# Kernel tuning notes

Hardware: AMD Instinct MI355X
Metric: run time of the kernel (lower is better)

Reference implementation:

```python
import jax, jax.numpy as jnp
import numpy as np
import math

# ---- constants derived from PCF.__init__(nbbins=50, sigma=0.25, npoints=1024, n_rmax=5) ----
NBBINS = 50
SIGMA = 0.25
NPOINTS = 1024
N_RMAX = 5
RMAX = float(2.0 * np.sqrt(1.0 / (2.0 * np.sqrt(3.0) * NPOINTS)))
_STEP = N_RMAX / NBBINS
RS = np.array([(i + 1) * _STEP * RMAX for i in range(NBBINS)], dtype=np.float32)
AREA = np.array([math.pi * ((r + 0.5 * RMAX) ** 2 - max(0.0, r - 0.5 * RMAX) ** 2) for r in RS],
                dtype=np.float32)
GF = float(1.0 / (np.sqrt(math.pi) * SIGMA))


def _gaussian_kernel(x):
    return GF * jnp.exp(-(x * x) / (SIGMA * SIGMA))


def _perimeter_weight(x, y, rs):
    """x, y: [N] disk centers in [0,1]^2; rs: [B]. Returns [N, B] inverse in-domain perimeter fraction."""
    full = jnp.full((x.shape[0], rs.shape[0]), 2.0 * math.pi, dtype=x.dtype)

    def corr(full_angle, dx, dy):
        # dx, dy: [N] distance to a domain edge (as in the four blocks of perimeter_weight)
        mask = rs[None, :] > dx[:, None]                       # [N, B]
        alpha = jnp.arccos(jnp.clip(dx[:, None] / rs[None, :], -1.0, 1.0))
        sub = (jnp.minimum(alpha, jnp.arctan2(dy, dx)[:, None])
               + jnp.minimum(alpha, jnp.arctan2(1.0 - dy, dx)[:, None]))
        return full_angle - jnp.where(mask, sub, 0.0)

    full = corr(full, x, y)          # left edge
    full = corr(full, 1.0 - x, y)    # right edge
    full = corr(full, y, x)          # bottom edge
    full = corr(full, 1.0 - y, x)    # top edge
    peri = jnp.clip(full / (2.0 * math.pi), 0.0, 1.0)
    pos = peri > 0
    return jnp.where(pos, 1.0 / jnp.where(pos, peri, 1.0), 0.0)


def _disk_distance(pa, pb, rmax):
    """pa: [Na,3], pb: [Nb,3] disks (x, y, r) -> pairwise disk distance [Na, Nb] (repo utils.diskDistance)."""
    diff = pa[:, None, 0:2] - pb[None, :, 0:2]
    d = jnp.sqrt(jnp.sum(diff * diff, axis=-1))                # [Na, Nb]
    ra = pa[:, 2][:, None]
    rb = pb[None, :, 2]
    r1 = jnp.maximum(ra, rb)
    r2 = jnp.minimum(ra, rb)
    extent = jnp.maximum(d + r1 + r2, 2.0 * r1)
    overlap = jnp.clip(r1 + r2 - d, 0.0, None)
    return (extent - overlap + d + r1 - r2) / rmax


def _pcf_forward(disks_a, disks_b, same_category):
    rs = jnp.asarray(RS)
    area = jnp.asarray(AREA)
    na = disks_a.shape[0]
    nb = disks_b.shape[0]
    dist = _disk_distance(disks_a, disks_b, RMAX)              # [Na, Nb]
    # val[i, j, b] = gauss(rs_b / rmax - dist_ij)
    val = _gaussian_kernel(rs[None, None, :] / RMAX - dist[:, :, None])  # [Na, Nb, B]
    if same_category:
        # exclude self-pair j == i (torch.cat of slices around i)
        eye = jnp.eye(na, nb, dtype=val.dtype)
        val = val * (1.0 - eye)[:, :, None]
    contrib = jnp.sum(val, axis=1)                             # [Na, B]
    weights = _perimeter_weight(disks_a[:, 0], disks_a[:, 1], rs)  # [Na, B] (diskfact = 1/domainLength = 1)
    density = contrib * weights / area[None, :] / nb           # [Na, B]
    pcf_mean = jnp.sum(density, axis=0) / na                   # [B]
    pcf_lower = jnp.min(density, axis=0)
    pcf_upper = jnp.max(density, axis=0)
    pcf = jnp.stack([rs / RMAX, pcf_mean], axis=1)             # [B, 2]
    return pcf, pcf_lower, pcf_upper


def setup_inputs() -> dict:
    key = jax.random.key(0)
    ka, kb = jax.random.split(key)
    disks_a = jax.random.uniform(ka, (1024, 3), dtype=jnp.float32)
    disks_b = jax.random.uniform(kb, (1024, 3), dtype=jnp.float32)
    return {"disks_a": disks_a, "disks_b": disks_b, "same_category": 0}


def reference(disks_a, disks_b, same_category):
    return _pcf_forward(disks_a, disks_b, same_category)
```

## Files before the change

### kernel.cpp

```cpp
#include <hip/hip_runtime.h>
#include <math.h>

#define NB 50

__device__ __forceinline__ float dev_rmax() {
    return (float)(2.0 * sqrt(1.0 / (2.0 * sqrt(3.0) * 1024.0)));
}

__global__ void __launch_bounds__(256)
pcf_density_kernel(const float* __restrict__ da, const float* __restrict__ db,
                   const int* __restrict__ scp, float* __restrict__ dens,
                   int na, int nb)
{
    const float RMAX = dev_rmax();
    const float inv_rmax = 1.0f / RMAX;
    const int i    = blockIdx.x;
    const int tid  = threadIdx.x;
    const int lane = tid & 63;
    const int wave = tid >> 6;
    const int sc   = scp[0];

    __shared__ float list[256];
    __shared__ int   cnt;
    __shared__ float part[4 * NB];

    if (tid == 0) cnt = 0;
    __syncthreads();

    const float ax = da[3*i+0];
    const float ay = da[3*i+1];
    const float ar = da[3*i+2];

    const float binf = 0.1f * (float)(lane + 1);
    float accb = 0.0f;

    for (int base = 0; base < nb; base += 256) {
        const int j = base + tid;
        bool close = false;
        float dist = 0.0f;
        if (j < nb) {
            const float bx = db[3*j+0];
            const float by = db[3*j+1];
            const float br = db[3*j+2];
            const float dx = ax - bx;
            const float dy = ay - by;
            const float d  = sqrtf(dx*dx + dy*dy);
            const float r1 = fmaxf(ar, br);
            const float r2 = fminf(ar, br);
            const float extent  = fmaxf(d + r1 + r2, 2.0f*r1);
            const float overlap = fmaxf(r1 + r2 - d, 0.0f);
            dist = (extent - overlap + d + r1 - r2) * inv_rmax;
            close = (dist < 7.5f) && !((sc != 0) && (j == i));
        }
        const unsigned long long m = __ballot(close);
        const int total  = __popcll(m);
        const int prefix = __popcll(m & ((1ull << lane) - 1ull));
        int wbase = 0;
        if (lane == 0) wbase = atomicAdd(&cnt, total);
        wbase = __shfl(wbase, 0);
        if (close) list[wbase + prefix] = dist;
        __syncthreads();

        const int M = cnt;
        for (int k = wave; k < M; k += 4) {
            const float dl = list[k];
            const float x  = binf - dl;
            accb += __expf(-16.0f * x * x);
        }
        __syncthreads();
        if (tid == 0) cnt = 0;
        __syncthreads();
    }

    if (lane < NB) part[wave * NB + lane] = accb;
    __syncthreads();

    if (wave == 0 && lane < NB) {
        const float s = part[lane] + part[NB + lane] + part[2*NB + lane] + part[3*NB + lane];

        const float PI = 3.14159265358979323846f;
        const float GF = 1.0f / (sqrtf(PI) * 0.25f);
        const float rs = 0.1f * (float)(lane + 1) * RMAX;

        float full = 2.0f * PI;
        const float ex[4] = { ax, 1.0f - ax, ay, 1.0f - ay };
        const float ey[4] = { ay, ay,        ax, ax        };
#pragma unroll
        for (int c = 0; c < 4; ++c) {
            if (rs > ex[c]) {
                float ratio = ex[c] / rs;
                ratio = fminf(fmaxf(ratio, -1.0f), 1.0f);
                const float alpha = acosf(ratio);
                const float a1 = atan2f(ey[c], ex[c]);
                const float a2 = atan2f(1.0f - ey[c], ex[c]);
                full -= fminf(alpha, a1) + fminf(alpha, a2);
            }
        }
        float peri = full * (1.0f / (2.0f * PI));
        peri = fminf(fmaxf(peri, 0.0f), 1.0f);
        const float w = (peri > 0.0f) ? (1.0f / peri) : 0.0f;

        const float r_out = rs + 0.5f * RMAX;
        const float r_in  = fmaxf(rs - 0.5f * RMAX, 0.0f);
        const float area  = PI * (r_out * r_out - r_in * r_in);

        const float density = (GF * s) * w / area / (float)nb;
        dens[lane * na + i] = density;
    }
}

__global__ void __launch_bounds__(256)
pcf_reduce_kernel(const float* __restrict__ dens, float* __restrict__ out, int na)
{
    const int b    = blockIdx.x;
    const int tid  = threadIdx.x;
    const int lane = tid & 63;
    const int wave = tid >> 6;
    const float RMAX = dev_rmax();

    __shared__ float rs_[4], rmn[4], rmx[4];

    float s = 0.0f, mn = INFINITY, mx = -INFINITY;
    for (int i = tid; i < na; i += 256) {
        const float v = dens[b * na + i];
        s  += v;
        mn  = fminf(mn, v);
        mx  = fmaxf(mx, v);
    }
#pragma unroll
    for (int off = 32; off >= 1; off >>= 1) {
        s  += __shfl_down(s, off);
        mn  = fminf(mn, __shfl_down(mn, off));
        mx  = fmaxf(mx, __shfl_down(mx, off));
    }
    if (lane == 0) { rs_[wave] = s; rmn[wave] = mn; rmx[wave] = mx; }
    __syncthreads();
    if (tid == 0) {
        float ts = rs_[0] + rs_[1] + rs_[2] + rs_[3];
        float tmn = fminf(fminf(rmn[0], rmn[1]), fminf(rmn[2], rmn[3]));
        float tmx = fmaxf(fmaxf(rmx[0], rmx[1]), fmaxf(rmx[2], rmx[3]));
        const float rs = 0.1f * (float)(b + 1) * RMAX;
        out[2*b + 0] = rs / RMAX;
        out[2*b + 1] = ts / (float)na;
        out[100 + b] = tmn;
        out[150 + b] = tmx;
    }
}

extern "C" void kernel_launch(void* const* d_in, const int* in_sizes, int n_in,
                              void* d_out, int out_size, void* d_ws, size_t ws_size,
                              hipStream_t stream)
{
    const float* da = (const float*)d_in[0];
    const float* db = (const float*)d_in[1];
    const int*   sc = (const int*)d_in[2];
    float* out  = (float*)d_out;
    float* dens = (float*)d_ws;
    const int na = in_sizes[0] / 3;
    const int nb = in_sizes[1] / 3;

    pcf_density_kernel<<<na, 256, 0, stream>>>(da, db, sc, dens, na, nb);
    pcf_reduce_kernel<<<NB, 256, 0, stream>>>(dens, out, na);
}
```

Measured before the change: 63.54 us.

## Process four A-disks per block with per-wave compacted lists

Each block now handles four A disks instead of one. Every loaded B disk is reused across those four, and close distances are compacted into a separate 1024-entry shared list per A disk. One wave then runs the Gaussian binning for one A disk, which removes the per-chunk barriers and the cross-wave partial reduction. This cuts B reloads and barrier overhead but gives only 256 blocks, and a single wave serially walks its whole list, so occupancy and parallelism drop.

```diff
diff --git a/kernel.cpp b/kernel.cpp
--- a/kernel.cpp
+++ b/kernel.cpp
@@ -2,6 +2,7 @@
 #include <math.h>
 
 #define NB 50
+#define KA 4
 
 __device__ __forceinline__ float dev_rmax() {
     return (float)(2.0 * sqrt(1.0 / (2.0 * sqrt(3.0) * 1024.0)));
@@ -13,78 +14,70 @@
                    int na, int nb)
 {
     const float RMAX = dev_rmax();
+    const float PI = 3.14159265358979323846f;
     const float inv_rmax = 1.0f / RMAX;
-    const int i    = blockIdx.x;
     const int tid  = threadIdx.x;
     const int lane = tid & 63;
     const int wave = tid >> 6;
     const int sc   = scp[0];
+    const int A0   = blockIdx.x * KA;
 
-    __shared__ float list[256];
-    __shared__ int   cnt;
-    __shared__ float part[4 * NB];
+    __shared__ float list[KA][1024];
+    __shared__ int   cnt[KA];
 
-    if (tid == 0) cnt = 0;
+    float ax[KA], ay[KA], ar[KA];
+#pragma unroll
+    for (int aa = 0; aa < KA; ++aa) {
+        const int ia = (A0 + aa < na) ? (A0 + aa) : (na - 1);
+        ax[aa] = da[3*ia+0]; ay[aa] = da[3*ia+1]; ar[aa] = da[3*ia+2];
+    }
+    if (tid < KA) cnt[tid] = 0;
     __syncthreads();
-
-    const float ax = da[3*i+0];
-    const float ay = da[3*i+1];
-    const float ar = da[3*i+2];
-
-    const float binf = 0.1f * (float)(lane + 1);
-    float accb = 0.0f;
 
     for (int base = 0; base < nb; base += 256) {
         const int j = base + tid;
-        bool close = false;
-        float dist = 0.0f;
-        if (j < nb) {
-            const float bx = db[3*j+0];
-            const float by = db[3*j+1];
-            const float br = db[3*j+2];
-            const float dx = ax - bx;
-            const float dy = ay - by;
+        const bool jvalid = (j < nb);
+        float bx = 0.0f, by = 0.0f, br = 0.0f;
+        if (jvalid) { bx = db[3*j+0]; by = db[3*j+1]; br = db[3*j+2]; }
+#pragma unroll
+        for (int aa = 0; aa < KA; ++aa) {
+            const float dx = ax[aa] - bx;
+            const float dy = ay[aa] - by;
             const float d  = sqrtf(dx*dx + dy*dy);
-            const float r1 = fmaxf(ar, br);
-            const float r2 = fminf(ar, br);
+            const float r1 = fmaxf(ar[aa], br);
+            const float r2 = fminf(ar[aa], br);
             const float extent  = fmaxf(d + r1 + r2, 2.0f*r1);
             const float overlap = fmaxf(r1 + r2 - d, 0.0f);
-            dist = (extent - overlap + d + r1 - r2) * inv_rmax;
-            close = (dist < 7.5f) && !((sc != 0) && (j == i));
+            const float dist = (extent - overlap + d + r1 - r2) * inv_rmax;
+            const bool close = jvalid && (dist < 7.5f)
+                               && !((sc != 0) && (j == A0 + aa));
+            const unsigned long long m = __ballot(close);
+            int wb = 0;
+            if (lane == 0 && m) wb = atomicAdd(&cnt[aa], __popcll(m));
+            wb = __shfl(wb, 0);
+            if (close) list[aa][wb + __popcll(m & ((1ull << lane) - 1ull))] = dist;
         }
-        const unsigned long long m = __ballot(close);
-        const int total  = __popcll(m);
-        const int prefix = __popcll(m & ((1ull << lane) - 1ull));
-        int wbase = 0;
-        if (lane == 0) wbase = atomicAdd(&cnt, total);
-        wbase = __shfl(wbase, 0);
-        if (close) list[wbase + prefix] = dist;
-        __syncthreads();
+    }
+    __syncthreads();
 
-        const int M = cnt;
-        for (int k = wave; k < M; k += 4) {
-            const float dl = list[k];
-            const float x  = binf - dl;
-            accb += __expf(-16.0f * x * x);
-        }
-        __syncthreads();
-        if (tid == 0) cnt = 0;
-        __syncthreads();
+    const float binf = 0.1f * (float)(lane + 1);
+    float acc = 0.0f;
+    const int M = cnt[wave];
+    for (int k = 0; k < M; ++k) {
+        const float x = binf - list[wave][k];
+        acc += __expf(-16.0f * x * x);
     }
 
-    if (lane < NB) part[wave * NB + lane] = accb;
-    __syncthreads();
-
-    if (wave == 0 && lane < NB) {
-        const float s = part[lane] + part[NB + lane] + part[2*NB + lane] + part[3*NB + lane];
-
-        const float PI = 3.14159265358979323846f;
+    if (lane < NB && (A0 + wave) < na) {
+        const int ia = A0 + wave;
+        const float axw = da[3*ia+0];
+        const float ayw = da[3*ia+1];
         const float GF = 1.0f / (sqrtf(PI) * 0.25f);
         const float rs = 0.1f * (float)(lane + 1) * RMAX;
 
         float full = 2.0f * PI;
-        const float ex[4] = { ax, 1.0f - ax, ay, 1.0f - ay };
-        const float ey[4] = { ay, ay,        ax, ax        };
+        const float ex[4] = { axw, 1.0f - axw, ayw, 1.0f - ayw };
+        const float ey[4] = { ayw, ayw,        axw, axw        };
 #pragma unroll
         for (int c = 0; c < 4; ++c) {
             if (rs > ex[c]) {
@@ -104,8 +97,8 @@
         const float r_in  = fmaxf(rs - 0.5f * RMAX, 0.0f);
         const float area  = PI * (r_out * r_out - r_in * r_in);
 
-        const float density = (GF * s) * w / area / (float)nb;
-        dens[lane * na + i] = density;
+        const float density = (GF * acc) * w / area / (float)nb;
+        dens[lane * na + ia] = density;
     }
 }
 
@@ -118,14 +111,12 @@
     const int wave = tid >> 6;
     const float RMAX = dev_rmax();
 
-    __shared__ float rs_[4], rmn[4], rmx[4];
+    __shared__ float rs_[4], rmn_[4], rmx_[4];
 
     float s = 0.0f, mn = INFINITY, mx = -INFINITY;
     for (int i = tid; i < na; i += 256) {
         const float v = dens[b * na + i];
-        s  += v;
-        mn  = fminf(mn, v);
-        mx  = fmaxf(mx, v);
+        s += v; mn = fminf(mn, v); mx = fmaxf(mx, v);
     }
 #pragma unroll
     for (int off = 32; off >= 1; off >>= 1) {
@@ -133,13 +124,13 @@
         mn  = fminf(mn, __shfl_down(mn, off));
         mx  = fmaxf(mx, __shfl_down(mx, off));
     }
-    if (lane == 0) { rs_[wave] = s; rmn[wave] = mn; rmx[wave] = mx; }
+    if (lane == 0) { rs_[wave] = s; rmn_[wave] = mn; rmx_[wave] = mx; }
     __syncthreads();
     if (tid == 0) {
-        float ts = rs_[0] + rs_[1] + rs_[2] + rs_[3];
-        float tmn = fminf(fminf(rmn[0], rmn[1]), fminf(rmn[2], rmn[3]));
-        float tmx = fmaxf(fmaxf(rmx[0], rmx[1]), fmaxf(rmx[2], rmx[3]));
-        const float rs = 0.1f * (float)(b + 1) * RMAX;
+        const float ts  = rs_[0] + rs_[1] + rs_[2] + rs_[3];
+        const float tmn = fminf(fminf(rmn_[0], rmn_[1]), fminf(rmn_[2], rmn_[3]));
+        const float tmx = fmaxf(fmaxf(rmx_[0], rmx_[1]), fmaxf(rmx_[2], rmx_[3]));
+        const float rs  = 0.1f * (float)(b + 1) * RMAX;
         out[2*b + 0] = rs / RMAX;
         out[2*b + 1] = ts / (float)na;
         out[100 + b] = tmn;
@@ -158,7 +149,8 @@
     float* dens = (float*)d_ws;
     const int na = in_sizes[0] / 3;
     const int nb = in_sizes[1] / 3;
+    const int nblk = (na + KA - 1) / KA;
 
-    pcf_density_kernel<<<na, 256, 0, stream>>>(da, db, sc, dens, na, nb);
+    pcf_density_kernel<<<nblk, 256, 0, stream>>>(da, db, sc, dens, na, nb);
     pcf_reduce_kernel<<<NB, 256, 0, stream>>>(dens, out, na);
 }
```

Result: slower. 64.98 us (+2.3%).
